# Kernel optimization log

Measured on AMD Instinct MI355X. Metric: run time of the kernel, lower is better.

The kernel has to match this reference:

```python
import jax, jax.numpy as jnp
import numpy as np

BT, D, H = 128, 256, 512

def setup_inputs() -> dict:
    key = jax.random.key(0)
    ks = jax.random.split(key, 15)
    f = jnp.float32
    n = lambda k, s, sc=1.0: jax.random.normal(k, s, dtype=f) * sc
    return {
        "x_t": n(ks[0], (BT, D)),
        "h1": n(ks[1], (BT, H)), "h2": n(ks[2], (BT, H)),
        "mnu1": n(ks[3], (BT, H), 0.1), "mnu2": n(ks[4], (BT, H), 0.1),
        "mth1": n(ks[5], (BT, H), 0.1), "mth2": n(ks[6], (BT, H), 0.1),
        "mw11": n(ks[7], (BT, D, H), 0.01), "mw12": n(ks[8], (BT, D, H), 0.01),
        "mw21": n(ks[9], (BT, D, H), 0.01), "mw22": n(ks[10], (BT, D, H), 0.01),
        "w1": n(ks[11], (D, H), 1.0 / np.sqrt(D)),
        "w2": n(ks[12], (D, H), 1.0 / np.sqrt(D)),
        "nu_log": n(ks[13], (H,), 0.5),
        "theta_log": n(ks[14], (H,), 0.5),
    }

def reference(x_t, h1, h2, mnu1, mnu2, mth1, mth2, mw11, mw12, mw21, mw22, w1, w2, nu_log, theta_log):
    # Linear RTU parametrization: r = exp(-exp(nu)), theta = exp(theta_log), gamma = sqrt(1 - r^2)
    exp_nu = jnp.exp(nu_log)
    r = jnp.exp(-exp_nu)                       # (H,)
    theta = jnp.exp(theta_log)
    g = jnp.sqrt(1.0 - r * r)
    A = r * jnp.cos(theta)                     # rotation matrix entries (H,)
    B = r * jnp.sin(theta)
    xw1 = x_t @ w1                             # (Bt, H)
    xw2 = x_t @ w2
    # hidden state update (complex rotation recurrence)
    c1 = A * h1 - B * h2 + g * xw1
    c2 = B * h1 + A * h2 + g * xw2
    # parameter sensitivities of A, B, g
    dA_dnu = -A * exp_nu
    dB_dnu = -B * exp_nu
    dg_dnu = (r * r) * exp_nu / g
    dA_dth = -B * theta
    dB_dth = A * theta
    # RTRL eligibility traces wrt nu_log: (Bt, H)
    n1 = A * mnu1 - B * mnu2 + dA_dnu * h1 - dB_dnu * h2 + dg_dnu * xw1
    n2 = B * mnu1 + A * mnu2 + dB_dnu * h1 + dA_dnu * h2 + dg_dnu * xw2
    # traces wrt theta_log: (Bt, H)
    t1 = A * mth1 - B * mth2 + dA_dth * h1 - dB_dth * h2
    t2 = B * mth1 + A * mth2 + dB_dth * h1 + dA_dth * h2
    # traces wrt W1/W2: (Bt, D, H); direct term gamma * x outer delta
    gx = g * x_t[:, :, None]                   # (Bt, D, H)
    W11 = A * mw11 - B * mw12 + gx
    W12 = B * mw11 + A * mw12
    W21 = A * mw21 - B * mw22
    W22 = B * mw21 + A * mw22 + gx
    h_t = jax.nn.relu(jnp.concatenate((c1, c2), axis=-1))  # (Bt, 2H)
    return (h_t, c1, c2, n1, n2, t1, t2, W11, W12, W21, W22)
```

## Files before the change

kernel.cpp:

```cpp
#include <hip/hip_runtime.h>

#define BT 128
#define D  256
#define H  512

#define OFF_HT  0
#define OFF_C1  131072
#define OFF_C2  196608
#define OFF_N1  262144
#define OFF_N2  327680
#define OFF_T1  393216
#define OFF_T2  458752
#define OFF_W11 524288
#define OFF_W12 17301504
#define OFF_W21 34078720
#define OFF_W22 50855936

#define SMALL_BLOCKS 256
#define BIG_ITER     8
#define BD_PER_BLOCK 16
#define BIG_BLOCKS   2048

typedef float f32x4 __attribute__((ext_vector_type(4)));

__global__ __launch_bounds__(256) void rtu_fused(
    const float*  __restrict__ x_t,
    const float*  __restrict__ h1,   const float* __restrict__ h2,
    const float*  __restrict__ mnu1, const float* __restrict__ mnu2,
    const float*  __restrict__ mth1, const float* __restrict__ mth2,
    const f32x4*  __restrict__ mw11, const f32x4* __restrict__ mw12,
    const f32x4*  __restrict__ mw21, const f32x4* __restrict__ mw22,
    const float*  __restrict__ w1,   const float* __restrict__ w2,
    const float*  __restrict__ nu_log, const float* __restrict__ theta_log,
    float* __restrict__ out)
{
    __shared__ float sA[H];
    __shared__ float sB[H];
    __shared__ float sG[H];
    __shared__ float xs[D];

    const int tid = threadIdx.x;

    if (blockIdx.x < SMALL_BLOCKS) {
        const int idx = blockIdx.x * 256 + tid;
        const int b   = idx >> 9;
        const int h   = idx & (H - 1);

        xs[tid] = x_t[b * D + tid];
        __syncthreads();

        const float exp_nu = expf(nu_log[h]);
        const float r      = expf(-exp_nu);
        const float theta  = expf(theta_log[h]);
        const float g      = sqrtf(fmaxf(1.0f - r * r, 0.0f));
        float s, c;
        sincosf(theta, &s, &c);
        const float A = r * c;
        const float B = r * s;
        const float dA_dnu = -A * exp_nu;
        const float dB_dnu = -B * exp_nu;
        const float dg_dnu = (r * r) * exp_nu / g;
        const float dA_dth = -B * theta;
        const float dB_dth =  A * theta;

        float xw1 = 0.0f, xw2 = 0.0f;
        #pragma unroll 8
        for (int d = 0; d < D; ++d) {
            const float xv = xs[d];
            xw1 = fmaf(xv, w1[d * H + h], xw1);
            xw2 = fmaf(xv, w2[d * H + h], xw2);
        }

        const float h1v = h1[idx],  h2v = h2[idx];
        const float mn1 = mnu1[idx], mn2 = mnu2[idx];
        const float mt1 = mth1[idx], mt2 = mth2[idx];

        const float c1v = A * h1v - B * h2v + g * xw1;
        const float c2v = B * h1v + A * h2v + g * xw2;

        const float n1v = A * mn1 - B * mn2 + dA_dnu * h1v - dB_dnu * h2v + dg_dnu * xw1;
        const float n2v = B * mn1 + A * mn2 + dB_dnu * h1v + dA_dnu * h2v + dg_dnu * xw2;

        const float t1v = A * mt1 - B * mt2 + dA_dth * h1v - dB_dth * h2v;
        const float t2v = B * mt1 + A * mt2 + dB_dth * h1v + dA_dth * h2v;

        out[OFF_HT + b * (2 * H) + h]     = fmaxf(c1v, 0.0f);
        out[OFF_HT + b * (2 * H) + H + h] = fmaxf(c2v, 0.0f);
        out[OFF_C1 + idx] = c1v;
        out[OFF_C2 + idx] = c2v;
        out[OFF_N1 + idx] = n1v;
        out[OFF_N2 + idx] = n2v;
        out[OFF_T1 + idx] = t1v;
        out[OFF_T2 + idx] = t2v;
        return;
    }

    #pragma unroll
    for (int i = 0; i < 2; ++i) {
        const int h = tid + i * 256;
        const float exp_nu = expf(nu_log[h]);
        const float r      = expf(-exp_nu);
        const float theta  = expf(theta_log[h]);
        float s, c;
        sincosf(theta, &s, &c);
        sA[h] = r * c;
        sB[h] = r * s;
        sG[h] = sqrtf(fmaxf(1.0f - r * r, 0.0f));
    }
    __syncthreads();

    const int hq = tid & 127;
    const int lr = tid >> 7;

    const f32x4 A4 = ((const f32x4*)sA)[hq];
    const f32x4 B4 = ((const f32x4*)sB)[hq];
    const f32x4 g4 = ((const f32x4*)sG)[hq];

    int bd = (blockIdx.x - SMALL_BLOCKS) * BD_PER_BLOCK + lr;

    f32x4* __restrict__ o11p = (f32x4*)(out + OFF_W11);
    f32x4* __restrict__ o12p = (f32x4*)(out + OFF_W12);
    f32x4* __restrict__ o21p = (f32x4*)(out + OFF_W21);
    f32x4* __restrict__ o22p = (f32x4*)(out + OFF_W22);

    #pragma unroll
    for (int it = 0; it < BIG_ITER; ++it, bd += 2) {
        const int e = bd * 128 + hq;

        const float x = x_t[bd];

        const f32x4 m11 = __builtin_nontemporal_load(mw11 + e);
        const f32x4 m12 = __builtin_nontemporal_load(mw12 + e);
        const f32x4 m21 = __builtin_nontemporal_load(mw21 + e);
        const f32x4 m22 = __builtin_nontemporal_load(mw22 + e);

        const f32x4 gx = g4 * x;

        f32x4 o11, o12, o21, o22;
        #pragma unroll
        for (int j = 0; j < 4; ++j) {
            o11[j] = fmaf(A4[j], m11[j], fmaf(-B4[j], m12[j], gx[j]));
            o12[j] = fmaf(B4[j], m11[j], A4[j] * m12[j]);
            o21[j] = fmaf(A4[j], m21[j], -B4[j] * m22[j]);
            o22[j] = fmaf(B4[j], m21[j], fmaf(A4[j], m22[j], gx[j]));
        }

        __builtin_nontemporal_store(o11, o11p + e);
        __builtin_nontemporal_store(o12, o12p + e);
        __builtin_nontemporal_store(o21, o21p + e);
        __builtin_nontemporal_store(o22, o22p + e);
    }
}

extern "C" void kernel_launch(void* const* d_in, const int* in_sizes, int n_in,
                              void* d_out, int out_size, void* d_ws, size_t ws_size,
                              hipStream_t stream) {
    const float* x_t   = (const float*)d_in[0];
    const float* h1    = (const float*)d_in[1];
    const float* h2    = (const float*)d_in[2];
    const float* mnu1  = (const float*)d_in[3];
    const float* mnu2  = (const float*)d_in[4];
    const float* mth1  = (const float*)d_in[5];
    const float* mth2  = (const float*)d_in[6];
    const float* mw11  = (const float*)d_in[7];
    const float* mw12  = (const float*)d_in[8];
    const float* mw21  = (const float*)d_in[9];
    const float* mw22  = (const float*)d_in[10];
    const float* w1    = (const float*)d_in[11];
    const float* w2    = (const float*)d_in[12];
    const float* nu_log    = (const float*)d_in[13];
    const float* theta_log = (const float*)d_in[14];

    float* out = (float*)d_out;

    rtu_fused<<<SMALL_BLOCKS + BIG_BLOCKS, 256, 0, stream>>>(
        x_t, h1, h2, mnu1, mnu2, mth1, mth2,
        (const f32x4*)mw11, (const f32x4*)mw12,
        (const f32x4*)mw21, (const f32x4*)mw22,
        w1, w2, nu_log, theta_log, out);
}
```

Measured before the change: 459.0 us.

## Split W-trace streams by half-block and software-prefetch next row

The big-block path now has each half of the block handle one of the two trace pairs (W11/W12 or W21/W22) across 16 consecutive (b,d) rows, instead of both halves interleaving rows while each thread touches all four arrays. Each thread keeps two input streams and two output streams, and the loads for the next row are issued explicitly before the current row is computed. The aim is fewer concurrent streams per thread and loads overlapped with compute in this bandwidth-bound kernel. In exchange, fewer loads are in flight per iteration unless the compiler hoists more of them, and each wave reads a longer contiguous span per array.

Result: no change. 458.1 us (-0.2%).

```diff
diff --git a/kernel.cpp b/kernel.cpp
--- a/kernel.cpp
+++ b/kernel.cpp
@@ -17,8 +17,7 @@
 #define OFF_W22 50855936
 
 #define SMALL_BLOCKS 256
-#define BIG_ITER     8
-#define BD_PER_BLOCK 16
+#define BIG_ITER     16
 #define BIG_BLOCKS   2048
 
 typedef float f32x4 __attribute__((ext_vector_type(4)));
@@ -109,46 +108,51 @@
     }
     __syncthreads();
 
-    const int hq = tid & 127;
-    const int lr = tid >> 7;
+    const int hq   = tid & 127;
+    const int pair = tid >> 7;
 
     const f32x4 A4 = ((const f32x4*)sA)[hq];
     const f32x4 B4 = ((const f32x4*)sB)[hq];
     const f32x4 g4 = ((const f32x4*)sG)[hq];
 
-    int bd = (blockIdx.x - SMALL_BLOCKS) * BD_PER_BLOCK + lr;
+    const f32x4 gF = pair ? (f32x4)(0.0f) : g4;
+    const f32x4 gS = pair ? g4 : (f32x4)(0.0f);
 
-    f32x4* __restrict__ o11p = (f32x4*)(out + OFF_W11);
-    f32x4* __restrict__ o12p = (f32x4*)(out + OFF_W12);
-    f32x4* __restrict__ o21p = (f32x4*)(out + OFF_W21);
-    f32x4* __restrict__ o22p = (f32x4*)(out + OFF_W22);
+    const int bd0 = (blockIdx.x - SMALL_BLOCKS) * BIG_ITER;
+
+    const f32x4* __restrict__ s0 = (pair ? mw21 : mw11) + bd0 * 128 + hq;
+    const f32x4* __restrict__ s1 = (pair ? mw22 : mw12) + bd0 * 128 + hq;
+    f32x4* __restrict__ d0 = (f32x4*)(out + (pair ? OFF_W21 : OFF_W11)) + bd0 * 128 + hq;
+    f32x4* __restrict__ d1 = (f32x4*)(out + (pair ? OFF_W22 : OFF_W12)) + bd0 * 128 + hq;
+
+    f32x4 a = __builtin_nontemporal_load(s0);
+    f32x4 b = __builtin_nontemporal_load(s1);
+    float x = x_t[bd0];
 
     #pragma unroll
-    for (int it = 0; it < BIG_ITER; ++it, bd += 2) {
-        const int e = bd * 128 + hq;
+    for (int it = 0; it < BIG_ITER; ++it) {
+        f32x4 an = a, bn = b;
+        float xn = x;
+        if (it + 1 < BIG_ITER) {
+            an = __builtin_nontemporal_load(s0 + (it + 1) * 128);
+            bn = __builtin_nontemporal_load(s1 + (it + 1) * 128);
+            xn = x_t[bd0 + it + 1];
+        }
 
-        const float x = x_t[bd];
+        const f32x4 gxf = gF * x;
+        const f32x4 gxs = gS * x;
 
-        const f32x4 m11 = __builtin_nontemporal_load(mw11 + e);
-        const f32x4 m12 = __builtin_nontemporal_load(mw12 + e);
-        const f32x4 m21 = __builtin_nontemporal_load(mw21 + e);
-        const f32x4 m22 = __builtin_nontemporal_load(mw22 + e);
-
-        const f32x4 gx = g4 * x;
-
-        f32x4 o11, o12, o21, o22;
+        f32x4 of, os;
         #pragma unroll
         for (int j = 0; j < 4; ++j) {
-            o11[j] = fmaf(A4[j], m11[j], fmaf(-B4[j], m12[j], gx[j]));
-            o12[j] = fmaf(B4[j], m11[j], A4[j] * m12[j]);
-            o21[j] = fmaf(A4[j], m21[j], -B4[j] * m22[j]);
-            o22[j] = fmaf(B4[j], m21[j], fmaf(A4[j], m22[j], gx[j]));
+            of[j] = fmaf(A4[j], a[j], fmaf(-B4[j], b[j], gxf[j]));
+            os[j] = fmaf(B4[j], a[j], fmaf(A4[j], b[j], gxs[j]));
         }
 
-        __builtin_nontemporal_store(o11, o11p + e);
-        __builtin_nontemporal_store(o12, o12p + e);
-        __builtin_nontemporal_store(o21, o21p + e);
-        __builtin_nontemporal_store(o22, o22p + e);
+        __builtin_nontemporal_store(of, d0 + it * 128);
+        __builtin_nontemporal_store(os, d1 + it * 128);
+
+        a = an; b = bn; x = xn;
     }
 }
 
```
